# Kernel tuning notes

Measured on AMD Instinct MI355X. Metric: run time of the kernel, lower is better.

## Reference

```python
import jax, jax.numpy as jnp
import numpy as np

B, T_ENC, T_DEC = 32, 512, 500
D_ENC = 512
N_MEL = 80 * 2  # mel_channels * mel_scale
K = 31          # location conv kernel size


def setup_inputs() -> dict:
    key = jax.random.key(0)
    ks = jax.random.split(key, 16)
    def w(k, shape, s=0.05):
        return jax.random.normal(k, shape, jnp.float32) * s
    z = lambda n: jnp.zeros((n,), jnp.float32)
    return {
        "encoder_out": w(ks[0], (B, T_ENC, D_ENC), 1.0),
        "mels": w(ks[1], (B, T_DEC, N_MEL), 1.0),
        "mask": jnp.zeros((B, 1, T_ENC), jnp.bool_),
        "w_pre1": w(ks[2], (256, N_MEL)), "b_pre1": z(256),
        "w_pre2": w(ks[3], (256, 256)), "b_pre2": z(256),
        "wih_a": w(ks[4], (4096, 256 + 512)), "whh_a": w(ks[5], (4096, 1024)),
        "bih_a": z(4096), "bhh_a": z(4096),
        "wq": w(ks[6], (128, 1024)), "bq": z(128),
        "wk": w(ks[7], (128, 512)), "bk": z(128),
        "conv_w": w(ks[8], (32, 2, K)), "conv_b": z(32),
        "wl": w(ks[9], (128, 32)), "bl": z(128),
        "wa": w(ks[10], (1, 128)), "ba": z(1),
        "wih_d": w(ks[11], (4096, 512 + 1024)), "whh_d": w(ks[12], (4096, 1024)),
        "bih_d": z(4096), "bhh_d": z(4096),
        "wm": w(ks[13], (N_MEL, 512 + 1024)), "bm": z(N_MEL),
        "wg": w(ks[14], (1, 512 + 1024)), "bg": z(1),
    }


def _lstm_cell(x, h, c, wih, whh, bih, bhh):
    g = x @ wih.T + bih + h @ whh.T + bhh
    i, f, gg, o = jnp.split(g, 4, axis=-1)
    c = jax.nn.sigmoid(f) * c + jax.nn.sigmoid(i) * jnp.tanh(gg)
    return jax.nn.sigmoid(o) * jnp.tanh(c), c


def _forward(encoder_out, mels, mask, w_pre1, b_pre1, w_pre2, b_pre2,
             wih_a, whh_a, bih_a, bhh_a, wq, bq, wk, bk, conv_w, conv_b,
             wl, bl, wa, ba, wih_d, whh_d, bih_d, bhh_d, wm, bm, wg, bg):
    b, t_enc, _ = encoder_out.shape
    n_mel = mels.shape[-1]
    mask1 = mask[:, 0, :]  # [B, T_enc], True = masked out
    # prepend zero frame, run prenet (ReLU MLP) over all frames at once
    mel_seq = jnp.concatenate([jnp.zeros((b, 1, n_mel), mels.dtype), mels], 1)
    pre = jax.nn.relu(mel_seq @ w_pre1.T + b_pre1)
    pre = jax.nn.relu(pre @ w_pre2.T + b_pre2)        # [B, T_dec+1, 256]
    pre = pre.transpose(1, 0, 2)                      # [T_dec+1, B, 256]
    mem_keys = encoder_out @ wk.T + bk                # [B, T_enc, 128]
    pad = K // 2

    def step(carry, mel_t):
        ctx, ah, ac, aw, awt, dh, dc = carry
        ah, ac = _lstm_cell(jnp.concatenate([mel_t, ctx], -1), ah, ac,
                            wih_a, whh_a, bih_a, bhh_a)
        query = ah @ wq.T + bq                        # [B, 128]
        fmap = jnp.stack([aw, awt], axis=1)           # [B, 2, T_enc]
        loc = jax.lax.conv_general_dilated(
            fmap, conv_w, (1,), [(pad, pad)],
            dimension_numbers=("NCH", "OIH", "NCH")) + conv_b[None, :, None]
        loc = loc.transpose(0, 2, 1) @ wl.T + bl      # [B, T_enc, 128]
        e = jnp.tanh(query[:, None, :] + mem_keys + loc) @ wa.T + ba  # [B,T_enc,1]
        e = jnp.where(mask1, -jnp.inf, e[..., 0])
        aw = jax.nn.softmax(e, -1)                    # [B, T_enc]
        awt = awt + aw
        ctx = jnp.einsum("bt,btd->bd", aw, encoder_out)
        dh, dc = _lstm_cell(jnp.concatenate([ctx, ah], -1), dh, dc,
                            wih_d, whh_d, bih_d, bhh_d)
        h = jnp.concatenate([dh, ctx], -1)            # [B, 1536]
        return (ctx, ah, ac, aw, awt, dh, dc), (h @ wm.T + bm, h @ wg.T + bg, aw)

    zf = lambda *s: jnp.zeros(s, encoder_out.dtype)
    carry0 = (zf(b, 512), zf(b, 1024), zf(b, 1024), zf(b, t_enc), zf(b, t_enc),
              zf(b, 1024), zf(b, 1024))
    _, (mels_out, gates_out, attn_out) = jax.lax.scan(step, carry0, pre)
    # mels_out [T_dec+1,B,n_mel], gates_out [T_dec+1,B,1], attn_out [T_dec+1,B,T_enc]
    return mels_out, gates_out, attn_out


def reference(encoder_out, mels, mask, w_pre1, b_pre1, w_pre2, b_pre2,
              wih_a, whh_a, bih_a, bhh_a, wq, bq, wk, bk, conv_w, conv_b,
              wl, bl, wa, ba, wih_d, whh_d, bih_d, bhh_d, wm, bm, wg, bg):
    return _forward(encoder_out, mels, mask, w_pre1, b_pre1, w_pre2, b_pre2,
                    wih_a, whh_a, bih_a, bhh_a, wq, bq, wk, bk, conv_w, conv_b,
                    wl, bl, wa, ba, wih_d, whh_d, bih_d, bhh_d, wm, bm, wg, bg)
```

## Files before the change

kernel.cpp:

```cpp
#include <hip/hip_runtime.h>
#include <hip/hip_bf16.h>


typedef __hip_bfloat16 bf16;

__device__ __forceinline__ float b2f(bf16 x){ return __bfloat162float(x); }
__device__ __forceinline__ bf16 f2b(float x){ return __float2bfloat16(x); }
__device__ __forceinline__ unsigned short f2bu(float x){
  union { bf16 h; unsigned short u; } cv; cv.h = __float2bfloat16(x); return cv.u;
}
__device__ __forceinline__ float us2f(unsigned short u){
  return __uint_as_float(((unsigned)u) << 16);
}
__device__ __forceinline__ float sig_s(float x){
  if (x > 30.f) return 1.f; if (x < -30.f) return 0.f;
  return 1.f/(1.f+__expf(-x)); }
__device__ __forceinline__ float tanh_s(float x){
  if (x > 15.f) return 1.f; if (x < -15.f) return -1.f;
  float e=__expf(2.f*x); return 1.f-2.f/(e+1.f); }

__device__ __forceinline__ float ld_cv(const float* p){
  return __hip_atomic_load(p, __ATOMIC_RELAXED, __HIP_MEMORY_SCOPE_AGENT);
}
__device__ __forceinline__ void st_cv(float* p, float v){
  __hip_atomic_store(p, v, __ATOMIC_RELAXED, __HIP_MEMORY_SCOPE_AGENT);
}
__device__ __forceinline__ float2 ld_cv2(const float* p){
  union { double d; float2 f; } u;
  u.d = __hip_atomic_load((const double*)p, __ATOMIC_RELAXED, __HIP_MEMORY_SCOPE_AGENT);
  return u.f;
}
__device__ __forceinline__ void st_cv2(float* p, float2 v){
  union { double d; float2 f; } u; u.f = v;
  __hip_atomic_store((double*)p, u.d, __ATOMIC_RELAXED, __HIP_MEMORY_SCOPE_AGENT);
}
__device__ __forceinline__ void at_add(float* p, float v){
  __hip_atomic_fetch_add(p, v, __ATOMIC_RELAXED, __HIP_MEMORY_SCOPE_AGENT);
}

constexpr size_t S_MKT   = 32ull*128*512;
constexpr size_t OFF_MKT = 0;
constexpr size_t OFF_AC  = OFF_MKT + S_MKT;
constexpr size_t OFF_DC  = OFF_AC + 32*1024;
constexpr size_t OFF_AW  = OFF_DC + 32*1024;
constexpr size_t OFF_AWT = OFF_AW + 32*512;
constexpr size_t OFF_BARS= OFF_AWT + 32*512;
constexpr size_t S_BARS  = 2560ull*288;
constexpr size_t OFF_GA  = OFF_BARS + S_BARS;
constexpr size_t OFF_GD  = OFF_GA + 32*4096;
constexpr size_t OFF_XA  = OFF_GD + 32*4096;
constexpr size_t ZERO_LEN = OFF_XA - OFF_AC;
constexpr size_t OFF_XD  = OFF_XA + 32*1792;
constexpr size_t OFF_RED = OFF_XD + 32*2560;
constexpr size_t OFF_BIASA = OFF_RED + 512;
constexpr size_t OFF_BIASD = OFF_BIASA + 4096;
constexpr size_t OFF_WFOLD = OFF_BIASD + 4096;
constexpr size_t OFF_QBIAS = OFF_WFOLD + 7936;
constexpr size_t OFF_WQT   = OFF_QBIAS + 128;
constexpr size_t OFF_F32_END = OFF_WQT + 1024*128;

constexpr size_t OFF_PRE2B_BYTES = ((OFF_F32_END*4 + 255)/256)*256;
constexpr size_t S_PRE2B = 501ull*32*256;
constexpr size_t OFF_WAT_BYTES = ((OFF_PRE2B_BYTES + S_PRE2B*2 + 255)/256)*256;
constexpr size_t S_WAT = 1792ull*4096;
constexpr size_t OFF_WDT_BYTES = OFF_WAT_BYTES + S_WAT*2;
constexpr size_t S_WDT = 2560ull*4096;
constexpr size_t WS_NEEDED = OFF_WDT_BYTES + S_WDT*2;

constexpr int LDS_WA = 57344;
constexpr int LDS_WD = 81920;
constexpr int LDS_SCR = 23552;
constexpr int SMEM_TOTAL = LDS_WA + LDS_WD + LDS_SCR;

constexpr size_t OUT_MEL  = 0;
constexpr size_t OUT_GATE = 501ull*32*160;
constexpr size_t OUT_ATTN = OUT_GATE + 501ull*32;

__global__ void k_zero(float* __restrict__ p, int n){
  int i = blockIdx.x*256 + threadIdx.x;
  if (i < n) p[i] = 0.f;
}

__global__ void k_bias(const float* __restrict__ b1, const float* __restrict__ b2,
                       float* __restrict__ out){
  int i = blockIdx.x*256 + threadIdx.x;
  if (i < 4096) out[i] = b1[i] + b2[i];
}

__global__ void k_fold(const float* __restrict__ cw, const float* __restrict__ cb,
                       const float* __restrict__ wl, const float* __restrict__ bl,
                       const float* __restrict__ bq,
                       float* __restrict__ wfold, float* __restrict__ qbias){
  int c = threadIdx.x;
  for (int kk = 0; kk < 62; ++kk){
    float a = 0.f;
    for (int o = 0; o < 32; ++o) a += wl[c*32 + o]*cw[o*62 + kk];
    wfold[c*62 + kk] = a;
  }
  float q = bq[c] + bl[c];
  for (int o = 0; o < 32; ++o) q += wl[c*32 + o]*cb[o];
  qbias[c] = q;
}

__global__ __launch_bounds__(256) void k_wqT(const float* __restrict__ wq,
                                             float* __restrict__ wqT){
  int idx = blockIdx.x*256 + threadIdx.x;
  int k = idx >> 7, c = idx & 127;
  wqT[idx] = wq[(size_t)c*1024 + k];
}

__global__ __launch_bounds__(256) void k_trans(const float* __restrict__ src, int C,
    unsigned short* __restrict__ dst, int koff, int CH, int SLICE){
  __shared__ unsigned short tile[64][65];
  int r0 = blockIdx.x*64, c0 = blockIdx.y*64;
  int tx = threadIdx.x & 63, ty = threadIdx.x >> 6;
  for (int rr = ty; rr < 64; rr += 4)
    tile[rr][tx] = f2bu(src[(size_t)(r0+rr)*C + c0 + tx]);
  __syncthreads();
  for (int rr = ty; rr < 64; rr += 4){
    int k = koff + c0 + rr;
    int kcc = k / CH, kl = k - kcc*CH;
    int j = r0 + tx, jtt = j >> 7, jl = j & 127;
    dst[(size_t)(kcc*32 + jtt)*SLICE + (size_t)(kl >> 2)*512 + jl*4 + (kl & 3)] = tile[tx][rr];
  }
}

__global__ __launch_bounds__(256) void k_prenet(const float* __restrict__ mels,
    const float* __restrict__ w1, const float* __restrict__ b1,
    const float* __restrict__ w2, const float* __restrict__ b2,
    bf16* __restrict__ pre2){
  __shared__ float mel[160];
  __shared__ float x1[256];
  int b = blockIdx.x, tid = threadIdx.x;
  for (int ti = 0; ti < 8; ++ti){
    int tt = blockIdx.y*8 + ti;
    if (tt >= 501) break;
    if (tid < 160) mel[tid] = (tt == 0) ? 0.f : mels[((size_t)b*500 + (tt-1))*160 + tid];
    __syncthreads();
    float a = b1[tid];
    for (int k = 0; k < 160; ++k) a += mel[k]*w1[tid*160 + k];
    x1[tid] = fmaxf(a, 0.f);
    __syncthreads();
    float a2 = b2[tid];
    for (int k = 0; k < 256; ++k) a2 += x1[k]*w2[tid*256 + k];
    pre2[((size_t)tt*32 + b)*256 + tid] = f2b(fmaxf(a2, 0.f));
    __syncthreads();
  }
}

__global__ __launch_bounds__(128) void k_memkeys(const float* __restrict__ enc,
    const float* __restrict__ wk, const float* __restrict__ bk, float* __restrict__ mkT){
  __shared__ float er[512];
  int b = blockIdx.x, tid = threadIdx.x;
  for (int i = 0; i < 8; ++i){
    int t = blockIdx.y*8 + i;
    const float* e = enc + ((size_t)b*512 + t)*512;
    for (int k = tid; k < 512; k += 128) er[k] = e[k];
    __syncthreads();
    float a = bk[tid];
    for (int k = 0; k < 512; ++k) a += er[k]*wk[tid*512 + k];
    mkT[((size_t)b*128 + tid)*512 + t] = a;
    __syncthreads();
  }
}

__device__ __forceinline__ void gridbar(unsigned* base){
  asm volatile("s_waitcnt vmcnt(0) lgkmcnt(0)" ::: "memory");
  __syncthreads();
  if (threadIdx.x == 0){
    unsigned* grp  = base + ((blockIdx.x >> 4) << 4);
    unsigned* root = base + 256;
    unsigned* go   = base + 272;
    if (__hip_atomic_fetch_add(grp, 1u, __ATOMIC_RELAXED, __HIP_MEMORY_SCOPE_AGENT) == 15u){
      if (__hip_atomic_fetch_add(root, 1u, __ATOMIC_RELAXED, __HIP_MEMORY_SCOPE_AGENT) == 15u)
        __hip_atomic_store(go, 1u, __ATOMIC_RELAXED, __HIP_MEMORY_SCOPE_AGENT);
    }
    while (!__hip_atomic_load(go, __ATOMIC_RELAXED, __HIP_MEMORY_SCOPE_AGENT))
      __builtin_amdgcn_s_sleep(4);
  }
  __syncthreads();
}

template<int CH, int KS, int HK>
__device__ __forceinline__ void gates_phase(const unsigned short* __restrict__ smW,
    float* xs, const float* xcat, float* G, int jt, int kc, int tid){
  const int jl = tid & 127, bg = tid >> 7;
  float acc[8];
  #pragma unroll
  for (int i = 0; i < 8; ++i) acc[i] = 0.f;
  const int k0 = kc*CH;
  for (int h = 0; h < CH/HK; ++h){
    __syncthreads();
    for (int i = tid; i < 16*HK; i += 512){
      int b = i/(HK/2), kp = i - b*(HK/2);
      ((float2*)xs)[i] = ld_cv2(xcat + (size_t)b*KS + k0 + h*HK + 2*kp);
    }
    __syncthreads();
    for (int kk = 0; kk < HK; kk += 4){
      const ushort4 w4 = *(const ushort4*)(smW + (size_t)((h*HK + kk) >> 2)*512 + jl*4);
      const float w0 = us2f(w4.x), w1 = us2f(w4.y), w2 = us2f(w4.z), w3 = us2f(w4.w);
      #pragma unroll
      for (int bb = 0; bb < 8; ++bb){
        const float4 xv = *(const float4*)&xs[(bg*8 + bb)*HK + kk];
        acc[bb] = fmaf(xv.x, w0, acc[bb]);
        acc[bb] = fmaf(xv.y, w1, acc[bb]);
        acc[bb] = fmaf(xv.z, w2, acc[bb]);
        acc[bb] = fmaf(xv.w, w3, acc[bb]);
      }
    }
  }
  #pragma unroll
  for (int bb = 0; bb < 8; ++bb)
    at_add(G + (size_t)(bg*8 + bb)*4096 + jt*128 + jl, acc[bb]);
}

__device__ __forceinline__ void cell_phase(float* G,
    const float* __restrict__ bias, float* cst,
    float* h0, int h0stride, int h0off,
    float* h1, int h1stride, int h1off,
    int blk, int tid){
  int idx = (blk*512 + tid)*2;
  int b = idx >> 10, u = idx & 1023;
  float* gb = G + (size_t)b*4096 + u;
  float2 gi = ld_cv2(gb), gf = ld_cv2(gb+1024), gg = ld_cv2(gb+2048), go = ld_cv2(gb+3072);
  float2 z = make_float2(0.f, 0.f);
  st_cv2(gb, z); st_cv2(gb+1024, z); st_cv2(gb+2048, z); st_cv2(gb+3072, z);
  gi.x += bias[u];      gi.y += bias[u+1];
  gf.x += bias[1024+u]; gf.y += bias[1024+u+1];
  gg.x += bias[2048+u]; gg.y += bias[2048+u+1];
  go.x += bias[3072+u]; go.y += bias[3072+u+1];
  float2 cp = *(const float2*)(cst + idx);
  float cn0 = sig_s(gf.x)*cp.x + sig_s(gi.x)*tanh_s(gg.x);
  float cn1 = sig_s(gf.y)*cp.y + sig_s(gi.y)*tanh_s(gg.y);
  float2 hh = make_float2(sig_s(go.x)*tanh_s(cn0), sig_s(go.y)*tanh_s(cn1));
  *(float2*)(cst + idx) = make_float2(cn0, cn1);
  st_cv2(h0 + (size_t)b*h0stride + h0off + u, hh);
  if (h1) st_cv2(h1 + (size_t)b*h1stride + h1off + u, hh);
}

__device__ __forceinline__ void out_proj_b(int b, int tid, int lane, int wv, int t,
    const float* xcatD, const float* __restrict__ wm,
    const float* __restrict__ bm, const float* __restrict__ wg,
    const float* __restrict__ bg,
    float* melOut, float* gateOut, float* xdS){
  for (int i = tid; i < 1280; i += 512)
    ((float2*)xdS)[i] = ld_cv2(xcatD + (size_t)b*2560 + 2*i);
  __syncthreads();
  for (int jo = wv; jo < 161; jo += 8){
    const float* wrow = (jo < 160) ? (wm + (size_t)jo*1536) : wg;
    float a = 0.f;
    for (int k = lane; k < 1536; k += 64){
      float x = (k < 1024) ? xdS[1536 + k] : xdS[k - 1024];
      a = fmaf(x, wrow[k], a);
    }
    #pragma unroll
    for (int off = 32; off; off >>= 1) a += __shfl_down(a, off, 64);
    if (lane == 0){
      if (jo < 160) melOut[((size_t)t*32 + b)*160 + jo] = a + bm[jo];
      else gateOut[t*32 + b] = a + bg[0];
    }
  }
}

__global__ __launch_bounds__(512) void k_decoder(
    const unsigned short* __restrict__ WaT, const unsigned short* __restrict__ WdT,
    const float* __restrict__ biasA, const float* __restrict__ biasD,
    const bf16* __restrict__ pre2b, const float* __restrict__ mkT,
    const float* __restrict__ enc, const unsigned char* __restrict__ mask,
    const float* __restrict__ wqT, const float* __restrict__ qbias,
    const float* __restrict__ wfold, const float* __restrict__ wa,
    const float* __restrict__ ba, const float* __restrict__ wm,
    const float* __restrict__ bm, const float* __restrict__ wg,
    const float* __restrict__ bg,
    float* xcatA, float* xcatD, float* ac, float* dc,
    float* aw, float* awt, float* GA, float* GD,
    float* redG, unsigned* bars,
    float* melOut, float* gateOut, float* attnOut)
{
  extern __shared__ __align__(16) char sm[];
  unsigned short* smWa = (unsigned short*)sm;
  unsigned short* smWd = (unsigned short*)(sm + LDS_WA);
  char* scr = sm + LDS_WA + LDS_WD;
  float* xs   = (float*)scr;
  float* xdS  = (float*)scr;
  float* ahS  = (float*)scr;
  float* qpP  = (float*)(scr + 4096);
  float* sqS  = (float*)(scr + 6144);
  float* eT   = (float*)(scr + 6656);
  float* sawL = (float*)(scr + 6912);
  float* s0   = (float*)(scr + 7168);
  float* s1   = (float*)(scr + 7552);

  const int blk = blockIdx.x, tid = threadIdx.x;
  const int lane = tid & 63, wv = tid >> 6;
  const int jt = blk & 31, kc = blk >> 5;

  {
    const ushort4* sa = (const ushort4*)(WaT + (size_t)(kc*32 + jt)*28672);
    ushort4* da = (ushort4*)smWa;
    for (int i = tid; i < 7168; i += 512) da[i] = sa[i];
    const ushort4* sd = (const ushort4*)(WdT + (size_t)(kc*32 + jt)*40960);
    ushort4* dd = (ushort4*)smWd;
    for (int i = tid; i < 10240; i += 512) dd[i] = sd[i];
  }
  for (int idx = blk*512 + tid; idx < 32*1792; idx += 131072){
    int b = idx / 1792, i = idx - b*1792;
    st_cv(xcatA + idx, (i < 256) ? b2f(pre2b[b*256 + i]) : 0.f);
  }
  for (int idx = blk*512 + tid; idx < 32*2560; idx += 131072) st_cv(xcatD + idx, 0.f);

  int bi = 0;
  gridbar(bars + (size_t)(bi++)*288);

  for (int t = 0; t < 501; ++t){
    gates_phase<224, 1792, 112>(smWa, xs, xcatA, GA, jt, kc, tid);
    if (blk < 32 && t > 0)
      cell_phase(GD, biasD, dc, xcatD, 2560, 1536, nullptr, 0, 0, blk, tid);
    gridbar(bars + (size_t)(bi++)*288);

    if (blk < 32){
      cell_phase(GA, biasA, ac, xcatA, 1792, 768, xcatD, 2560, 512, blk, tid);
    } else if (blk >= 64 && blk < 96){
      if (t > 0)
        out_proj_b(blk-64, tid, lane, wv, t-1, xcatD, wm, bm, wg, bg,
                   melOut, gateOut, xdS);
    } else if (blk >= 96 && blk < 128){
      if (t < 500){
        int b = blk - 96;
        const bf16* ps = pre2b + ((size_t)(t+1)*32 + b)*256;
        for (int i = tid; i < 128; i += 512)
          st_cv2(xcatA + (size_t)b*1792 + 2*i,
                 make_float2(b2f(ps[2*i]), b2f(ps[2*i+1])));
      }
    }
    gridbar(bars + (size_t)(bi++)*288);

    {
      int b = blk >> 3, tt = blk & 7, t0 = tt*64;
      if (tid < 32){
        float2 z = make_float2(0.f, 0.f);
        st_cv2(xcatA + (size_t)b*1792 + 256 + t0 + 2*tid, z);
        st_cv2(xcatD + (size_t)b*2560 + t0 + 2*tid, z);
      }
      for (int i = tid; i < 188; i += 512){
        int ch = (i >= 94), p2 = ch ? i-94 : i;
        int pos = t0 + p2 - 15;
        float v = (pos >= 0 && pos < 512)
                ? (ch ? ld_cv(awt + b*512 + pos) : ld_cv(aw + b*512 + pos)) : 0.f;
        (ch ? s1 : s0)[p2] = v;
      }
      if (tid < 512)
        ((float2*)ahS)[tid] = ld_cv2(xcatA + (size_t)b*1792 + 768 + 2*tid);
      __syncthreads();
      {
        int c = tid & 127, kq = tid >> 7;
        const float* ap = ahS + kq*256;
        const float* wp = wqT + (size_t)(kq*256)*128 + c;
        float p = 0.f;
        for (int k = 0; k < 256; ++k) p = fmaf(ap[k], wp[(size_t)k*128], p);
        qpP[kq*128 + c] = p;
      }
      __syncthreads();
      if (tid < 128)
        sqS[tid] = qpP[tid] + qpP[128+tid] + qpP[256+tid] + qpP[384+tid] + qbias[tid];
      __syncthreads();
      int tl = tid & 63, cg = tid >> 6;
      const float* mkb = mkT + (size_t)b*65536 + t0 + tl;
      float a = 0.f;
      for (int ci = 0; ci < 16; ++ci){
        int c = cg*16 + ci;
        const float* wf = wfold + c*62;
        float lc = 0.f;
        #pragma unroll
        for (int k = 0; k < 31; ++k)
          lc = fmaf(wf[k], s0[tl+k], fmaf(wf[31+k], s1[tl+k], lc));
        float s = sqS[c] + mkb[(size_t)c*512] + lc;
        a = fmaf(tanh_s(s), wa[c], a);
      }
      qpP[cg*64 + tl] = a;
      __syncthreads();
      if (tid < 64){
        float e = ba[0];
        #pragma unroll
        for (int g = 0; g < 8; ++g) e += qpP[g*64 + tid];
        if (mask[b*512 + t0 + tid]) e = -1e30f;
        eT[tid] = e;
        float m = e;
        #pragma unroll
        for (int off = 32; off; off >>= 1) m = fmaxf(m, __shfl_xor(m, off, 64));
        float pe = __expf(e - m), ss = pe;
        #pragma unroll
        for (int off = 32; off; off >>= 1) ss += __shfl_xor(ss, off, 64);
        if (tid == 0)
          st_cv2(redG + (size_t)(b*8 + tt)*2, make_float2(m, ss));
      }
    }
    gridbar(bars + (size_t)(bi++)*288);

    {
      int b = blk >> 3, tt = blk & 7, t0 = tt*64;
      if (tid < 64){
        float M = -1e30f, S = 0.f;
        float2 ms[8];
        #pragma unroll
        for (int i = 0; i < 8; ++i){
          ms[i] = ld_cv2(redG + (size_t)(b*8 + i)*2);
          M = fmaxf(M, ms[i].x);
        }
        #pragma unroll
        for (int i = 0; i < 8; ++i) S += ms[i].y*__expf(ms[i].x - M);
        float av = __expf(eT[tid] - M)/S;
        int tg = t0 + tid;
        st_cv(aw + b*512 + tg, av);
        st_cv(awt + b*512 + tg, ld_cv(awt + b*512 + tg) + av);
        attnOut[((size_t)t*32 + b)*512 + tg] = av;
        sawL[tid] = av;
      }
      __syncthreads();
      {
        float accd = 0.f;
        const float* eb = enc + ((size_t)b*512 + t0)*512 + tid;
        for (int tau = 0; tau < 64; ++tau) accd = fmaf(sawL[tau], eb[(size_t)tau*512], accd);
        at_add(xcatA + (size_t)b*1792 + 256 + tid, accd);
        at_add(xcatD + (size_t)b*2560 + tid, accd);
      }
    }
    gridbar(bars + (size_t)(bi++)*288);

    gates_phase<320, 2560, 160>(smWd, xs, xcatD, GD, jt, kc, tid);
    gridbar(bars + (size_t)(bi++)*288);
  }

  if (blk < 32)
    cell_phase(GD, biasD, dc, xcatD, 2560, 1536, nullptr, 0, 0, blk, tid);
  gridbar(bars + (size_t)(bi++)*288);
  if (blk < 32)
    out_proj_b(blk, tid, lane, wv, 500, xcatD, wm, bm, wg, bg, melOut, gateOut, xdS);
}

extern "C" void kernel_launch(void* const* d_in, const int* in_sizes, int n_in,
                              void* d_out, int out_size, void* d_ws, size_t ws_size,
                              hipStream_t stream){
  if (ws_size < WS_NEEDED) return;

  const float* enc    = (const float*)d_in[0];
  const float* mels   = (const float*)d_in[1];
  const unsigned char* mask = (const unsigned char*)d_in[2];
  const float* w_pre1 = (const float*)d_in[3];
  const float* b_pre1 = (const float*)d_in[4];
  const float* w_pre2 = (const float*)d_in[5];
  const float* b_pre2 = (const float*)d_in[6];
  const float* wih_a  = (const float*)d_in[7];
  const float* whh_a  = (const float*)d_in[8];
  const float* bih_a  = (const float*)d_in[9];
  const float* bhh_a  = (const float*)d_in[10];
  const float* wq     = (const float*)d_in[11];
  const float* bq     = (const float*)d_in[12];
  const float* wk     = (const float*)d_in[13];
  const float* bk     = (const float*)d_in[14];
  const float* conv_w = (const float*)d_in[15];
  const float* conv_b = (const float*)d_in[16];
  const float* wl     = (const float*)d_in[17];
  const float* bl     = (const float*)d_in[18];
  const float* wa     = (const float*)d_in[19];
  const float* ba     = (const float*)d_in[20];
  const float* wih_d  = (const float*)d_in[21];
  const float* whh_d  = (const float*)d_in[22];
  const float* bih_d  = (const float*)d_in[23];
  const float* bhh_d  = (const float*)d_in[24];
  const float* wm     = (const float*)d_in[25];
  const float* bm     = (const float*)d_in[26];
  const float* wg     = (const float*)d_in[27];
  const float* bg     = (const float*)d_in[28];

  float* W = (float*)d_ws;
  float* mkT   = W + OFF_MKT;
  float* ac    = W + OFF_AC;
  float* dc    = W + OFF_DC;
  float* aw    = W + OFF_AW;
  float* awt   = W + OFF_AWT;
  unsigned* bars = (unsigned*)(W + OFF_BARS);
  float* GA    = W + OFF_GA;
  float* GD    = W + OFF_GD;
  float* xcatA = W + OFF_XA;
  float* xcatD = W + OFF_XD;
  float* redG  = W + OFF_RED;
  float* biasA = W + OFF_BIASA;
  float* biasD = W + OFF_BIASD;
  float* wfold = W + OFF_WFOLD;
  float* qbias = W + OFF_QBIAS;
  float* wqT   = W + OFF_WQT;
  unsigned short* WaT = (unsigned short*)((char*)d_ws + OFF_WAT_BYTES);
  unsigned short* WdT = (unsigned short*)((char*)d_ws + OFF_WDT_BYTES);
  bf16* pre2b = (bf16*)((char*)d_ws + OFF_PRE2B_BYTES);

  float* out    = (float*)d_out;
  float* melOut = out + OUT_MEL;
  float* gateOut= out + OUT_GATE;
  float* attnOut= out + OUT_ATTN;

  static int smem_set = 0;
  if (!smem_set){
    hipFuncSetAttribute((const void*)k_decoder,
                        hipFuncAttributeMaxDynamicSharedMemorySize, SMEM_TOTAL);
    smem_set = 1;
  }

  k_zero<<<(int)((ZERO_LEN + 255)/256), 256, 0, stream>>>(W + OFF_AC, (int)ZERO_LEN);
  k_bias<<<16, 256, 0, stream>>>(bih_a, bhh_a, biasA);
  k_bias<<<16, 256, 0, stream>>>(bih_d, bhh_d, biasD);
  k_fold<<<1, 128, 0, stream>>>(conv_w, conv_b, wl, bl, bq, wfold, qbias);
  k_wqT<<<512, 256, 0, stream>>>(wq, wqT);
  k_trans<<<dim3(64, 12), 256, 0, stream>>>(wih_a, 768,  WaT, 0,    224, 28672);
  k_trans<<<dim3(64, 16), 256, 0, stream>>>(whh_a, 1024, WaT, 768,  224, 28672);
  k_trans<<<dim3(64, 24), 256, 0, stream>>>(wih_d, 1536, WdT, 0,    320, 40960);
  k_trans<<<dim3(64, 16), 256, 0, stream>>>(whh_d, 1024, WdT, 1536, 320, 40960);
  k_prenet<<<dim3(32, 63), 256, 0, stream>>>(mels, w_pre1, b_pre1, w_pre2, b_pre2, pre2b);
  k_memkeys<<<dim3(32, 64), 128, 0, stream>>>(enc, wk, bk, mkT);

  k_decoder<<<256, 512, SMEM_TOTAL, stream>>>(WaT, WdT, biasA, biasD, pre2b, mkT, enc, mask,
                                              wqT, qbias, wfold, wa, ba, wm, bm, wg, bg,
                                              xcatA, xcatD, ac, dc, aw, awt,
                                              GA, GD, redG, bars,
                                              melOut, gateOut, attnOut);
}
```

Baseline: 169.9 ms.

## Use bf16 copies of encoder/query/output weights and XCD-aware block roles with per-XCD barrier flags

Converts the encoder output, the query weight and the mel/gate projection weights to bf16 copies in the workspace, so the persistent decoder streams half the bytes in its context, query and output-projection loops. Remaps block roles and attention batch assignment using blk&7 so each role's work is spread across XCDs. The grid barrier now releases through eight separate go flags, one per XCD, each on its own cache line, so spinning blocks do not all poll one line; the sleep interval is doubled. Adds conversion kernels, lowers the precision of those operands, and adds coherent load/store variants for cell state and outputs.

```diff
diff --git a/kernel.cpp b/kernel.cpp
--- a/kernel.cpp
+++ b/kernel.cpp
@@ -38,14 +38,13 @@
   __hip_atomic_fetch_add(p, v, __ATOMIC_RELAXED, __HIP_MEMORY_SCOPE_AGENT);
 }
 
-constexpr size_t S_MKT   = 32ull*128*512;
 constexpr size_t OFF_MKT = 0;
-constexpr size_t OFF_AC  = OFF_MKT + S_MKT;
+constexpr size_t OFF_AC  = OFF_MKT + 32ull*128*512;
 constexpr size_t OFF_DC  = OFF_AC + 32*1024;
 constexpr size_t OFF_AW  = OFF_DC + 32*1024;
 constexpr size_t OFF_AWT = OFF_AW + 32*512;
 constexpr size_t OFF_BARS= OFF_AWT + 32*512;
-constexpr size_t S_BARS  = 2560ull*288;
+constexpr size_t S_BARS  = 2560ull*512;
 constexpr size_t OFF_GA  = OFF_BARS + S_BARS;
 constexpr size_t OFF_GD  = OFF_GA + 32*4096;
 constexpr size_t OFF_XA  = OFF_GD + 32*4096;
@@ -56,8 +55,7 @@
 constexpr size_t OFF_BIASD = OFF_BIASA + 4096;
 constexpr size_t OFF_WFOLD = OFF_BIASD + 4096;
 constexpr size_t OFF_QBIAS = OFF_WFOLD + 7936;
-constexpr size_t OFF_WQT   = OFF_QBIAS + 128;
-constexpr size_t OFF_F32_END = OFF_WQT + 1024*128;
+constexpr size_t OFF_F32_END = OFF_QBIAS + 128;
 
 constexpr size_t OFF_PRE2B_BYTES = ((OFF_F32_END*4 + 255)/256)*256;
 constexpr size_t S_PRE2B = 501ull*32*256;
@@ -65,7 +63,13 @@
 constexpr size_t S_WAT = 1792ull*4096;
 constexpr size_t OFF_WDT_BYTES = OFF_WAT_BYTES + S_WAT*2;
 constexpr size_t S_WDT = 2560ull*4096;
-constexpr size_t WS_NEEDED = OFF_WDT_BYTES + S_WDT*2;
+constexpr size_t OFF_ENCB_BYTES = OFF_WDT_BYTES + S_WDT*2;
+constexpr size_t S_ENCB = 32ull*512*512;
+constexpr size_t OFF_WQTB_BYTES = OFF_ENCB_BYTES + S_ENCB*2;
+constexpr size_t S_WQTB = 1024ull*128;
+constexpr size_t OFF_WMB_BYTES = OFF_WQTB_BYTES + S_WQTB*2;
+constexpr size_t S_WMB = 161ull*1536;
+constexpr size_t WS_NEEDED = OFF_WMB_BYTES + S_WMB*2;
 
 constexpr int LDS_WA = 57344;
 constexpr int LDS_WD = 81920;
@@ -102,11 +106,27 @@
   qbias[c] = q;
 }
 
-__global__ __launch_bounds__(256) void k_wqT(const float* __restrict__ wq,
-                                             float* __restrict__ wqT){
+__global__ __launch_bounds__(256) void k_wqTb(const float* __restrict__ wq,
+                                              unsigned short* __restrict__ wqTb){
   int idx = blockIdx.x*256 + threadIdx.x;
   int k = idx >> 7, c = idx & 127;
-  wqT[idx] = wq[(size_t)c*1024 + k];
+  wqTb[idx] = f2bu(wq[(size_t)c*1024 + k]);
+}
+
+__global__ __launch_bounds__(256) void k_wmb(const float* __restrict__ wm,
+                                             const float* __restrict__ wg,
+                                             unsigned short* __restrict__ wmb){
+  int idx = blockIdx.x*256 + threadIdx.x;
+  if (idx >= 161*1536) return;
+  int r = idx / 1536, k = idx - r*1536;
+  wmb[idx] = f2bu(r < 160 ? wm[(size_t)r*1536 + k] : wg[k]);
+}
+
+__global__ __launch_bounds__(256) void k_encb(const float* __restrict__ enc,
+                                              unsigned short* __restrict__ encB){
+  for (size_t i = (size_t)blockIdx.x*256 + threadIdx.x; i < S_ENCB;
+       i += (size_t)gridDim.x*256)
+    encB[i] = f2bu(enc[i]);
 }
 
 __global__ __launch_bounds__(256) void k_trans(const float* __restrict__ src, int C,
@@ -164,19 +184,23 @@
   }
 }
 
-__device__ __forceinline__ void gridbar(unsigned* base){
+__device__ __forceinline__ void gridbar(unsigned* base, int xcd){
   asm volatile("s_waitcnt vmcnt(0) lgkmcnt(0)" ::: "memory");
   __syncthreads();
   if (threadIdx.x == 0){
     unsigned* grp  = base + ((blockIdx.x >> 4) << 4);
     unsigned* root = base + 256;
-    unsigned* go   = base + 272;
     if (__hip_atomic_fetch_add(grp, 1u, __ATOMIC_RELAXED, __HIP_MEMORY_SCOPE_AGENT) == 15u){
-      if (__hip_atomic_fetch_add(root, 1u, __ATOMIC_RELAXED, __HIP_MEMORY_SCOPE_AGENT) == 15u)
-        __hip_atomic_store(go, 1u, __ATOMIC_RELAXED, __HIP_MEMORY_SCOPE_AGENT);
-    }
+      if (__hip_atomic_fetch_add(root, 1u, __ATOMIC_RELAXED, __HIP_MEMORY_SCOPE_AGENT) == 15u){
+        #pragma unroll
+        for (int x = 0; x < 8; ++x)
+          __hip_atomic_store(base + 288 + x*16, 1u,
+                             __ATOMIC_RELAXED, __HIP_MEMORY_SCOPE_AGENT);
+      }
+    }
+    unsigned* go = base + 288 + xcd*16;
     while (!__hip_atomic_load(go, __ATOMIC_RELAXED, __HIP_MEMORY_SCOPE_AGENT))
-      __builtin_amdgcn_s_sleep(4);
+      __builtin_amdgcn_s_sleep(8);
   }
   __syncthreads();
 }
@@ -218,8 +242,8 @@
     const float* __restrict__ bias, float* cst,
     float* h0, int h0stride, int h0off,
     float* h1, int h1stride, int h1off,
-    int blk, int tid){
-  int idx = (blk*512 + tid)*2;
+    int ord, int tid){
+  int idx = (ord*512 + tid)*2;
   int b = idx >> 10, u = idx & 1023;
   float* gb = G + (size_t)b*4096 + u;
   float2 gi = ld_cv2(gb), gf = ld_cv2(gb+1024), gg = ld_cv2(gb+2048), go = ld_cv2(gb+3072);
@@ -229,35 +253,34 @@
   gf.x += bias[1024+u]; gf.y += bias[1024+u+1];
   gg.x += bias[2048+u]; gg.y += bias[2048+u+1];
   go.x += bias[3072+u]; go.y += bias[3072+u+1];
-  float2 cp = *(const float2*)(cst + idx);
+  float2 cp = ld_cv2(cst + idx);
   float cn0 = sig_s(gf.x)*cp.x + sig_s(gi.x)*tanh_s(gg.x);
   float cn1 = sig_s(gf.y)*cp.y + sig_s(gi.y)*tanh_s(gg.y);
   float2 hh = make_float2(sig_s(go.x)*tanh_s(cn0), sig_s(go.y)*tanh_s(cn1));
-  *(float2*)(cst + idx) = make_float2(cn0, cn1);
+  st_cv2(cst + idx, make_float2(cn0, cn1));
   st_cv2(h0 + (size_t)b*h0stride + h0off + u, hh);
   if (h1) st_cv2(h1 + (size_t)b*h1stride + h1off + u, hh);
 }
 
 __device__ __forceinline__ void out_proj_b(int b, int tid, int lane, int wv, int t,
-    const float* xcatD, const float* __restrict__ wm,
-    const float* __restrict__ bm, const float* __restrict__ wg,
-    const float* __restrict__ bg,
+    const float* xcatD, const unsigned short* __restrict__ wmb,
+    const float* __restrict__ bm, const float* __restrict__ bg,
     float* melOut, float* gateOut, float* xdS){
   for (int i = tid; i < 1280; i += 512)
     ((float2*)xdS)[i] = ld_cv2(xcatD + (size_t)b*2560 + 2*i);
   __syncthreads();
   for (int jo = wv; jo < 161; jo += 8){
-    const float* wrow = (jo < 160) ? (wm + (size_t)jo*1536) : wg;
+    const unsigned short* wrow = wmb + (size_t)jo*1536;
     float a = 0.f;
     for (int k = lane; k < 1536; k += 64){
       float x = (k < 1024) ? xdS[1536 + k] : xdS[k - 1024];
-      a = fmaf(x, wrow[k], a);
+      a = fmaf(x, us2f(wrow[k]), a);
     }
     #pragma unroll
     for (int off = 32; off; off >>= 1) a += __shfl_down(a, off, 64);
     if (lane == 0){
-      if (jo < 160) melOut[((size_t)t*32 + b)*160 + jo] = a + bm[jo];
-      else gateOut[t*32 + b] = a + bg[0];
+      if (jo < 160) st_cv(melOut + ((size_t)t*32 + b)*160 + jo, a + bm[jo]);
+      else st_cv(gateOut + t*32 + b, a + bg[0]);
     }
   }
 }
@@ -266,12 +289,11 @@
     const unsigned short* __restrict__ WaT, const unsigned short* __restrict__ WdT,
     const float* __restrict__ biasA, const float* __restrict__ biasD,
     const bf16* __restrict__ pre2b, const float* __restrict__ mkT,
-    const float* __restrict__ enc, const unsigned char* __restrict__ mask,
-    const float* __restrict__ wqT, const float* __restrict__ qbias,
+    const unsigned short* __restrict__ encB, const unsigned char* __restrict__ mask,
+    const unsigned short* __restrict__ wqTb, const float* __restrict__ qbias,
     const float* __restrict__ wfold, const float* __restrict__ wa,
-    const float* __restrict__ ba, const float* __restrict__ wm,
-    const float* __restrict__ bm, const float* __restrict__ wg,
-    const float* __restrict__ bg,
+    const float* __restrict__ ba, const unsigned short* __restrict__ wmb,
+    const float* __restrict__ bm, const float* __restrict__ bg,
     float* xcatA, float* xcatD, float* ac, float* dc,
     float* aw, float* awt, float* GA, float* GD,
     float* redG, unsigned* bars,
@@ -294,6 +316,12 @@
   const int blk = blockIdx.x, tid = threadIdx.x;
   const int lane = tid & 63, wv = tid >> 6;
   const int jt = blk & 31, kc = blk >> 5;
+  const int xcd  = blk & 7;
+  const int loc8 = blk >> 3;
+  const int batt = xcd*4 + (loc8 & 3);
+  const int ttat = loc8 >> 2;
+  const int role = loc8 >> 2;
+  const int ord  = xcd*4 + (loc8 & 3);
 
   {
     const ushort4* sa = (const ushort4*)(WaT + (size_t)(kc*32 + jt)*28672);
@@ -310,33 +338,31 @@
   for (int idx = blk*512 + tid; idx < 32*2560; idx += 131072) st_cv(xcatD + idx, 0.f);
 
   int bi = 0;
-  gridbar(bars + (size_t)(bi++)*288);
+  gridbar(bars + (size_t)(bi++)*512, xcd);
 
   for (int t = 0; t < 501; ++t){
     gates_phase<224, 1792, 112>(smWa, xs, xcatA, GA, jt, kc, tid);
-    if (blk < 32 && t > 0)
-      cell_phase(GD, biasD, dc, xcatD, 2560, 1536, nullptr, 0, 0, blk, tid);
-    gridbar(bars + (size_t)(bi++)*288);
-
-    if (blk < 32){
-      cell_phase(GA, biasA, ac, xcatA, 1792, 768, xcatD, 2560, 512, blk, tid);
-    } else if (blk >= 64 && blk < 96){
+    if (role == 0 && t > 0)
+      cell_phase(GD, biasD, dc, xcatD, 2560, 1536, nullptr, 0, 0, ord, tid);
+    gridbar(bars + (size_t)(bi++)*512, xcd);
+
+    if (role == 0){
+      cell_phase(GA, biasA, ac, xcatA, 1792, 768, xcatD, 2560, 512, ord, tid);
+    } else if (role == 1){
       if (t > 0)
-        out_proj_b(blk-64, tid, lane, wv, t-1, xcatD, wm, bm, wg, bg,
-                   melOut, gateOut, xdS);
-    } else if (blk >= 96 && blk < 128){
+        out_proj_b(ord, tid, lane, wv, t-1, xcatD, wmb, bm, bg, melOut, gateOut, xdS);
+    } else if (role == 2){
       if (t < 500){
-        int b = blk - 96;
-        const bf16* ps = pre2b + ((size_t)(t+1)*32 + b)*256;
+        const bf16* ps = pre2b + ((size_t)(t+1)*32 + ord)*256;
         for (int i = tid; i < 128; i += 512)
-          st_cv2(xcatA + (size_t)b*1792 + 2*i,
+          st_cv2(xcatA + (size_t)ord*1792 + 2*i,
                  make_float2(b2f(ps[2*i]), b2f(ps[2*i+1])));
       }
     }
-    gridbar(bars + (size_t)(bi++)*288);
+    gridbar(bars + (size_t)(bi++)*512, xcd);
 
     {
-      int b = blk >> 3, tt = blk & 7, t0 = tt*64;
+      int b = batt, t0 = ttat*64;
       if (tid < 32){
         float2 z = make_float2(0.f, 0.f);
         st_cv2(xcatA + (size_t)b*1792 + 256 + t0 + 2*tid, z);
@@ -349,15 +375,14 @@
                 ? (ch ? ld_cv(awt + b*512 + pos) : ld_cv(aw + b*512 + pos)) : 0.f;
         (ch ? s1 : s0)[p2] = v;
       }
-      if (tid < 512)
-        ((float2*)ahS)[tid] = ld_cv2(xcatA + (size_t)b*1792 + 768 + 2*tid);
+      ((float2*)ahS)[tid] = ld_cv2(xcatA + (size_t)b*1792 + 768 + 2*tid);
       __syncthreads();
       {
         int c = tid & 127, kq = tid >> 7;
         const float* ap = ahS + kq*256;
-        const float* wp = wqT + (size_t)(kq*256)*128 + c;
+        const unsigned short* wp = wqTb + (size_t)(kq*256)*128 + c;
         float p = 0.f;
-        for (int k = 0; k < 256; ++k) p = fmaf(ap[k], wp[(size_t)k*128], p);
+        for (int k = 0; k < 256; ++k) p = fmaf(ap[k], us2f(wp[(size_t)k*128]), p);
         qpP[kq*128 + c] = p;
       }
       __syncthreads();
@@ -392,13 +417,13 @@
         #pragma unroll
         for (int off = 32; off; off >>= 1) ss += __shfl_xor(ss, off, 64);
         if (tid == 0)
-          st_cv2(redG + (size_t)(b*8 + tt)*2, make_float2(m, ss));
-      }
-    }
-    gridbar(bars + (size_t)(bi++)*288);
+          st_cv2(redG + (size_t)(b*8 + ttat)*2, make_float2(m, ss));
+      }
+    }
+    gridbar(bars + (size_t)(bi++)*512, xcd);
 
     {
-      int b = blk >> 3, tt = blk & 7, t0 = tt*64;
+      int b = batt, t0 = ttat*64;
       if (tid < 64){
         float M = -1e30f, S = 0.f;
         float2 ms[8];
@@ -413,29 +438,30 @@
         int tg = t0 + tid;
         st_cv(aw + b*512 + tg, av);
         st_cv(awt + b*512 + tg, ld_cv(awt + b*512 + tg) + av);
-        attnOut[((size_t)t*32 + b)*512 + tg] = av;
+        st_cv(attnOut + ((size_t)t*32 + b)*512 + tg, av);
         sawL[tid] = av;
       }
       __syncthreads();
       {
         float accd = 0.f;
-        const float* eb = enc + ((size_t)b*512 + t0)*512 + tid;
-        for (int tau = 0; tau < 64; ++tau) accd = fmaf(sawL[tau], eb[(size_t)tau*512], accd);
+        const unsigned short* eb = encB + ((size_t)b*512 + t0)*512 + tid;
+        for (int tau = 0; tau < 64; ++tau)
+          accd = fmaf(sawL[tau], us2f(eb[(size_t)tau*512]), accd);
         at_add(xcatA + (size_t)b*1792 + 256 + tid, accd);
         at_add(xcatD + (size_t)b*2560 + tid, accd);
       }
     }
-    gridbar(bars + (size_t)(bi++)*288);
+    gridbar(bars + (size_t)(bi++)*512, xcd);
 
     gates_phase<320, 2560, 160>(smWd, xs, xcatD, GD, jt, kc, tid);
-    gridbar(bars + (size_t)(bi++)*288);
-  }
-
-  if (blk < 32)
-    cell_phase(GD, biasD, dc, xcatD, 2560, 1536, nullptr, 0, 0, blk, tid);
-  gridbar(bars + (size_t)(bi++)*288);
-  if (blk < 32)
-    out_proj_b(blk, tid, lane, wv, 500, xcatD, wm, bm, wg, bg, melOut, gateOut, xdS);
+    gridbar(bars + (size_t)(bi++)*512, xcd);
+  }
+
+  if (role == 0)
+    cell_phase(GD, biasD, dc, xcatD, 2560, 1536, nullptr, 0, 0, ord, tid);
+  gridbar(bars + (size_t)(bi++)*512, xcd);
+  if (role == 1)
+    out_proj_b(ord, tid, lane, wv, 500, xcatD, wmb, bm, bg, melOut, gateOut, xdS);
 }
 
 extern "C" void kernel_launch(void* const* d_in, const int* in_sizes, int n_in,
@@ -489,9 +515,11 @@
   float* biasD = W + OFF_BIASD;
   float* wfold = W + OFF_WFOLD;
   float* qbias = W + OFF_QBIAS;
-  float* wqT   = W + OFF_WQT;
-  unsigned short* WaT = (unsigned short*)((char*)d_ws + OFF_WAT_BYTES);
-  unsigned short* WdT = (unsigned short*)((char*)d_ws + OFF_WDT_BYTES);
+  unsigned short* WaT  = (unsigned short*)((char*)d_ws + OFF_WAT_BYTES);
+  unsigned short* WdT  = (unsigned short*)((char*)d_ws + OFF_WDT_BYTES);
+  unsigned short* encB = (unsigned short*)((char*)d_ws + OFF_ENCB_BYTES);
+  unsigned short* wqTb = (unsigned short*)((char*)d_ws + OFF_WQTB_BYTES);
+  unsigned short* wmb  = (unsigned short*)((char*)d_ws + OFF_WMB_BYTES);
   bf16* pre2b = (bf16*)((char*)d_ws + OFF_PRE2B_BYTES);
 
   float* out    = (float*)d_out;
@@ -510,7 +538,9 @@
   k_bias<<<16, 256, 0, stream>>>(bih_a, bhh_a, biasA);
   k_bias<<<16, 256, 0, stream>>>(bih_d, bhh_d, biasD);
   k_fold<<<1, 128, 0, stream>>>(conv_w, conv_b, wl, bl, bq, wfold, qbias);
-  k_wqT<<<512, 256, 0, stream>>>(wq, wqT);
+  k_wqTb<<<512, 256, 0, stream>>>(wq, wqTb);
+  k_wmb<<<966, 256, 0, stream>>>(wm, wg, wmb);
+  k_encb<<<2048, 256, 0, stream>>>(enc, encB);
   k_trans<<<dim3(64, 12), 256, 0, stream>>>(wih_a, 768,  WaT, 0,    224, 28672);
   k_trans<<<dim3(64, 16), 256, 0, stream>>>(whh_a, 1024, WaT, 768,  224, 28672);
   k_trans<<<dim3(64, 24), 256, 0, stream>>>(wih_d, 1536, WdT, 0,    320, 40960);
@@ -518,8 +548,9 @@
   k_prenet<<<dim3(32, 63), 256, 0, stream>>>(mels, w_pre1, b_pre1, w_pre2, b_pre2, pre2b);
   k_memkeys<<<dim3(32, 64), 128, 0, stream>>>(enc, wk, bk, mkT);
 
-  k_decoder<<<256, 512, SMEM_TOTAL, stream>>>(WaT, WdT, biasA, biasD, pre2b, mkT, enc, mask,
-                                              wqT, qbias, wfold, wa, ba, wm, bm, wg, bg,
+  k_decoder<<<256, 512, SMEM_TOTAL, stream>>>(WaT, WdT, biasA, biasD, pre2b, mkT,
+                                              encB, mask, wqTb, qbias, wfold, wa, ba,
+                                              wmb, bm, bg,
                                               xcatA, xcatD, ac, dc, aw, awt,
                                               GA, GD, redG, bars,
                                               melOut, gateOut, attnOut);
```

Measured after the change: 162.9 ms. 1.04x faster.
